# Kernel tuning notes

Hardware: AMD Instinct MI355X
Metric: run time of the kernel (lower is better)

## Reference

```python
import jax, jax.numpy as jnp
import numpy as np

N, F_IN, HID, C = 50000, 256, 64, 40
E = 1_600_000
EPS = 1e-8  # torch cosine_similarity eps


def setup_inputs() -> dict:
    key = jax.random.key(0)
    ks = jax.random.split(key, 6)
    x = jax.random.normal(ks[0], (N, F_IN), jnp.float32)
    edge_index = jax.random.randint(ks[1], (2, E), 0, N, dtype=jnp.int64)
    edge_weights = jax.random.uniform(ks[2], (E,), jnp.float32)
    W1 = jax.random.normal(ks[3], (F_IN, HID), jnp.float32) / np.float32(np.sqrt(F_IN))
    b1 = jnp.zeros((HID,), jnp.float32)
    W2 = jax.random.normal(ks[4], (HID, C), jnp.float32) / np.float32(np.sqrt(HID))
    b2 = jnp.zeros((C,), jnp.float32)
    return {"x": x, "edge_index": edge_index, "edge_weights": edge_weights,
            "W1": W1, "b1": b1, "W2": W2, "b2": b2}


def _gcn_conv(x, W, b, src, dst, n):
    # PyG GCNConv: out = D^{-1/2} (A + I) D^{-1/2} (X W) + b
    xw = x @ W  # [n, out]
    loops = jnp.arange(n, dtype=src.dtype)
    s = jnp.concatenate([src, loops])  # self-loops appended
    d = jnp.concatenate([dst, loops])
    deg = jax.ops.segment_sum(jnp.ones_like(s, dtype=xw.dtype), d, num_segments=n)
    dinv = jnp.where(deg > 0, jax.lax.rsqrt(jnp.maximum(deg, 1.0)), 0.0)
    norm = dinv[s] * dinv[d]  # [E+n]
    msg = xw[s] * norm[:, None]  # gather + scale (irregular access)
    out = jax.ops.segment_sum(msg, d, num_segments=n)  # scatter-add
    return out + b


def reference(x, edge_index, edge_weights, W1, b1, W2, b2):
    src, dst = edge_index[0], edge_index[1]
    n = x.shape[0]
    # layer 1 + relu (dropout = identity in eval)
    h = jax.nn.relu(_gcn_conv(x, W1, b1, src, dst, n))
    x_out = _gcn_conv(h, W2, b2, src, dst, n)  # [n, C]
    # edge-wise cosine dissimilarity: 1 - cos(x_out[src], x_out[dst])
    a = x_out[src]
    b = x_out[dst]
    na = jnp.maximum(jnp.sqrt(jnp.sum(a * a, axis=-1)), EPS)
    nb = jnp.maximum(jnp.sqrt(jnp.sum(b * b, axis=-1)), EPS)
    cosine_sim = 1.0 - jnp.sum(a * b, axis=-1) / (na * nb)
    gnn_edge = jnp.where(edge_weights > 0.5, 1.0, -1.0)
    return (jax.nn.log_softmax(x_out, axis=1), x_out, cosine_sim, gnn_edge,
            jax.nn.softmax(x_out, axis=1))
```

## Files before the change

### kernel.cpp

```cpp
#include <hip/hip_runtime.h>
#include <hip/hip_bf16.h>

#define F_IN 256
#define HID  64
#define CLS  40
#define EPS  1e-8f
#define XS_STRIDE 264
#define EPB  8192

typedef unsigned short ushort_t;
typedef unsigned int   uint_t;
typedef __attribute__((ext_vector_type(8))) short bf16x8;
typedef __attribute__((ext_vector_type(4))) float f32x4;

__device__ __forceinline__ float bf2f(ushort_t u) {
    union { uint_t i; float f; } v; v.i = ((uint_t)u) << 16; return v.f;
}
__device__ __forceinline__ ushort_t f2bf(float f) {
    union { float f; uint_t i; } v; v.f = f;
    uint_t r = v.i + 0x7fff + ((v.i >> 16) & 1);
    return (ushort_t)(r >> 16);
}
__device__ __forceinline__ float blo(uint_t p) {
    union { uint_t i; float f; } v; v.i = p << 16; return v.f;
}
__device__ __forceinline__ float bhi(uint_t p) {
    union { uint_t i; float f; } v; v.i = p & 0xffff0000u; return v.f;
}
__device__ __forceinline__ float dot_u4(uint4 a, uint4 b) {
    return blo(a.x) * blo(b.x) + bhi(a.x) * bhi(b.x)
         + blo(a.y) * blo(b.y) + bhi(a.y) * bhi(b.y)
         + blo(a.z) * blo(b.z) + bhi(a.z) * bhi(b.z)
         + blo(a.w) * blo(b.w) + bhi(a.w) * bhi(b.w);
}

__global__ void detect_kernel(const int* __restrict__ raw, int* __restrict__ flag) {
    int c = threadIdx.x;
    int w = raw[2 * c + 1];
    unsigned long long b = __ballot(w != 0);
    if (c == 0) *flag = (b == 0ULL) ? 1 : 0;
}

__global__ void build_hist_kernel(const void* __restrict__ raw, const int* __restrict__ flag,
                                  uint_t* __restrict__ pair, int* __restrict__ ghist, int E) {
    __shared__ int lhist[256];
    int tid = threadIdx.x;
    lhist[tid] = 0;
    __syncthreads();
    int base = blockIdx.x * EPB;
    if (*flag) {
        const long long* r = (const long long*)raw;
        for (int it = 0; it < EPB / 1024; ++it) {
            int e = base + (it * 256 + tid) * 4;
            if (e + 4 <= E) {
                ulonglong2 a0 = *(const ulonglong2*)(r + e);
                ulonglong2 a1 = *(const ulonglong2*)(r + e + 2);
                ulonglong2 b0 = *(const ulonglong2*)(r + E + e);
                ulonglong2 b1 = *(const ulonglong2*)(r + E + e + 2);
                uint_t d0 = (uint_t)b0.x, d1 = (uint_t)b0.y;
                uint_t d2 = (uint_t)b1.x, d3 = (uint_t)b1.y;
                uint4 p;
                p.x = (d0 << 16) | (uint_t)a0.x;
                p.y = (d1 << 16) | (uint_t)a0.y;
                p.z = (d2 << 16) | (uint_t)a1.x;
                p.w = (d3 << 16) | (uint_t)a1.y;
                *(uint4*)(pair + e) = p;
                atomicAdd(&lhist[d0 >> 8], 1);
                atomicAdd(&lhist[d1 >> 8], 1);
                atomicAdd(&lhist[d2 >> 8], 1);
                atomicAdd(&lhist[d3 >> 8], 1);
            } else {
                for (int k = 0; k < 4; ++k) {
                    int ee = e + k;
                    if (ee < E) {
                        uint_t s = (uint_t)r[ee];
                        uint_t d = (uint_t)r[E + ee];
                        pair[ee] = (d << 16) | s;
                        atomicAdd(&lhist[d >> 8], 1);
                    }
                }
            }
        }
    } else {
        const int* r = (const int*)raw;
        for (int it = 0; it < EPB / 1024; ++it) {
            int e = base + (it * 256 + tid) * 4;
            if (e + 4 <= E) {
                int4 a = *(const int4*)(r + e);
                int4 b = *(const int4*)(r + E + e);
                uint_t d0 = (uint_t)b.x, d1 = (uint_t)b.y;
                uint_t d2 = (uint_t)b.z, d3 = (uint_t)b.w;
                uint4 p;
                p.x = (d0 << 16) | (uint_t)a.x;
                p.y = (d1 << 16) | (uint_t)a.y;
                p.z = (d2 << 16) | (uint_t)a.z;
                p.w = (d3 << 16) | (uint_t)a.w;
                *(uint4*)(pair + e) = p;
                atomicAdd(&lhist[d0 >> 8], 1);
                atomicAdd(&lhist[d1 >> 8], 1);
                atomicAdd(&lhist[d2 >> 8], 1);
                atomicAdd(&lhist[d3 >> 8], 1);
            } else {
                for (int k = 0; k < 4; ++k) {
                    int ee = e + k;
                    if (ee < E) {
                        uint_t s = (uint_t)r[ee];
                        uint_t d = (uint_t)r[E + ee];
                        pair[ee] = (d << 16) | s;
                        atomicAdd(&lhist[d >> 8], 1);
                    }
                }
            }
        }
    }
    __syncthreads();
    ghist[blockIdx.x * 256 + tid] = lhist[tid];
}

__global__ void scan_cols_kernel(int* __restrict__ ghist, int* __restrict__ btot,
                                 int NBLK) {
    int k    = blockIdx.x;
    int lane = threadIdx.x;
    int carry = 0;
    for (int b0 = 0; b0 < NBLK; b0 += 64) {
        int b = b0 + lane;
        int v = (b < NBLK) ? ghist[b * 256 + k] : 0;
        int x = v;
        #pragma unroll
        for (int o = 1; o < 64; o <<= 1) {
            int t = __shfl_up(x, o);
            if (lane >= o) x += t;
        }
        if (b < NBLK) ghist[b * 256 + k] = carry + x - v;
        carry += __shfl(x, 63);
    }
    if (lane == 0) btot[k] = carry;
}

__global__ void scan_base_kernel(const int* __restrict__ btot, int* __restrict__ bbase) {
    __shared__ int s[256];
    int k = threadIdx.x;
    int v = btot[k];
    int x = v;
    s[k] = x;
    __syncthreads();
    #pragma unroll
    for (int o = 1; o < 256; o <<= 1) {
        int t = (k >= o) ? s[k - o] : 0;
        __syncthreads();
        x += t;
        s[k] = x;
        __syncthreads();
    }
    bbase[k] = x - v;
    if (k == 255) bbase[256] = x;
}

__global__ void scatter_buckets_kernel(const uint_t* __restrict__ pair,
                                       const int* __restrict__ ghist,
                                       const int* __restrict__ bbase,
                                       uint_t* __restrict__ bkt, int E) {
    __shared__ int cursor[256];
    int tid = threadIdx.x;
    cursor[tid] = ghist[blockIdx.x * 256 + tid] + bbase[tid];
    __syncthreads();
    int base = blockIdx.x * EPB;
    for (int it = 0; it < EPB / 256; ++it) {
        int e = base + it * 256 + tid;
        if (e < E) {
            uint_t u = pair[e];
            int pos = atomicAdd(&cursor[u >> 24], 1);
            bkt[pos] = u;
        }
    }
}

__global__ void bucket_csr_kernel(const uint_t* __restrict__ bkt,
                                  const int* __restrict__ bbase,
                                  ushort_t* __restrict__ csr, int* __restrict__ rowptr,
                                  float* __restrict__ dinv, int n, int E, int NBUCK) {
    __shared__ int lhist[256];
    __shared__ int lscan[256];
    __shared__ int cursor[256];
    int tid = threadIdx.x;
    int kb  = blockIdx.x;
    int base = bbase[kb];
    int cnt  = bbase[kb + 1] - base;
    lhist[tid] = 0;
    __syncthreads();
    for (int i = tid; i < cnt; i += 256) {
        uint_t u = bkt[base + i];
        atomicAdd(&lhist[(u >> 16) & 255], 1);
    }
    __syncthreads();
    int v = lhist[tid];
    int x = v;
    lscan[tid] = x;
    __syncthreads();
    #pragma unroll
    for (int o = 1; o < 256; o <<= 1) {
        int t = (tid >= o) ? lscan[tid - o] : 0;
        __syncthreads();
        x += t;
        lscan[tid] = x;
        __syncthreads();
    }
    int excl = x - v;
    int node = kb * 256 + tid;
    if (node < n) {
        rowptr[node] = base + excl;
        dinv[node]   = rsqrtf((float)(v + 1));
    }
    cursor[tid] = base + excl;
    if (kb == NBUCK - 1 && tid == 0) rowptr[n] = E;
    __syncthreads();
    for (int i = tid; i < cnt; i += 256) {
        uint_t u = bkt[base + i];
        int pos = atomicAdd(&cursor[(u >> 16) & 255], 1);
        csr[pos] = (ushort_t)(u & 0xffffu);
    }
}

__global__ void convert_w1_kernel(const float* __restrict__ W1, ushort_t* __restrict__ W1s) {
    int t = blockIdx.x * blockDim.x + threadIdx.x;
    if (t >= 4 * 8 * 64) return;
    int lane = t & 63;
    int kk   = (t >> 6) & 7;
    int nt   = t >> 9;
    int col  = nt * 16 + (lane & 15);
    int k0   = kk * 32 + (lane >> 4) * 8;
    ushort_t v[8];
    #pragma unroll
    for (int j = 0; j < 8; ++j) v[j] = f2bf(W1[(size_t)(k0 + j) * HID + col]);
    uint4 p;
    p.x = (uint_t)v[0] | ((uint_t)v[1] << 16);
    p.y = (uint_t)v[2] | ((uint_t)v[3] << 16);
    p.z = (uint_t)v[4] | ((uint_t)v[5] << 16);
    p.w = (uint_t)v[6] | ((uint_t)v[7] << 16);
    *(uint4*)(W1s + (size_t)t * 8) = p;
}

__global__ void gemm1_mfma_kernel(const float* __restrict__ x,
                                  const ushort_t* __restrict__ W1s,
                                  const float* __restrict__ dinv,
                                  ushort_t* __restrict__ xws, int n) {
    __shared__ ushort_t xs[16 * XS_STRIDE];
    int node0 = blockIdx.x * 16;
    int tid = threadIdx.x;
    for (int i = tid; i < 16 * 64; i += 256) {
        int r  = i >> 6;
        int c4 = (i & 63) << 2;
        int node = node0 + r;
        float4 v = (node < n) ? *(const float4*)(x + (size_t)node * F_IN + c4)
                              : make_float4(0.f, 0.f, 0.f, 0.f);
        ushort4 b;
        b.x = f2bf(v.x); b.y = f2bf(v.y); b.z = f2bf(v.z); b.w = f2bf(v.w);
        *(ushort4*)(&xs[r * XS_STRIDE + c4]) = b;
    }
    __syncthreads();
    int wave = tid >> 6;
    int lane = tid & 63;
    int m    = lane & 15;
    int q    = lane >> 4;
    f32x4 acc = {0.f, 0.f, 0.f, 0.f};
    #pragma unroll
    for (int kk = 0; kk < 8; ++kk) {
        bf16x8 a = *(const bf16x8*)(&xs[m * XS_STRIDE + kk * 32 + q * 8]);
        bf16x8 b = *(const bf16x8*)(W1s + (((size_t)wave * 8 + kk) * 64 + lane) * 8);
        acc = __builtin_amdgcn_mfma_f32_16x16x32_bf16(a, b, acc, 0, 0, 0);
    }
    int ch = wave * 16 + m;
    #pragma unroll
    for (int r = 0; r < 4; ++r) {
        int node = node0 + q * 4 + r;
        if (node < n)
            xws[(size_t)node * HID + ch] = f2bf(acc[r] * dinv[node]);
    }
}

__global__ void gather1_gemm2_kernel(const int* __restrict__ rowptr,
                                     const ushort_t* __restrict__ csr,
                                     const ushort_t* __restrict__ xws,
                                     const float* __restrict__ dinv,
                                     const float* __restrict__ b1,
                                     const float* __restrict__ W2,
                                     ushort_t* __restrict__ hws, int n) {
    __shared__ float hbuf[4][72];
    __shared__ float w2s[HID * CLS];
    int tid  = threadIdx.x;
    int wave = tid >> 6;
    int l    = tid & 63;
    int g    = l >> 3;
    int lc   = l & 7;
    for (int i = tid; i < HID * CLS / 4; i += 256)
        *(float4*)(&w2s[i * 4]) = *(const float4*)(W2 + i * 4);
    int wv = (blockIdx.x * blockDim.x + tid) >> 6;
    bool active = wv < n;
    int beg = 0, endp = 0;
    float di = 0.f;
    float acc8[8];
    #pragma unroll
    for (int j = 0; j < 8; ++j) acc8[j] = 0.f;
    if (active) {
        beg = rowptr[wv]; endp = rowptr[wv + 1];
        di  = dinv[wv];
        if (l < 8) {
            uint4 sv = *(const uint4*)(xws + (size_t)wv * HID + lc * 8);
            acc8[0] = blo(sv.x); acc8[1] = bhi(sv.x);
            acc8[2] = blo(sv.y); acc8[3] = bhi(sv.y);
            acc8[4] = blo(sv.z); acc8[5] = bhi(sv.z);
            acc8[6] = blo(sv.w); acc8[7] = bhi(sv.w);
        }
    }
    for (int ch = beg; ch < endp; ch += 32) {
        #pragma unroll
        for (int k = 0; k < 4; ++k) {
            int e = ch + k * 8 + g;
            bool val = e < endp;
            int ec = val ? e : (endp - 1);
            int s = (int)csr[ec];
            uint4 p = *(const uint4*)(xws + (size_t)s * HID + lc * 8);
            if (!val) { p.x = 0u; p.y = 0u; p.z = 0u; p.w = 0u; }
            acc8[0] += blo(p.x); acc8[1] += bhi(p.x);
            acc8[2] += blo(p.y); acc8[3] += bhi(p.y);
            acc8[4] += blo(p.z); acc8[5] += bhi(p.z);
            acc8[6] += blo(p.w); acc8[7] += bhi(p.w);
        }
    }
    #pragma unroll
    for (int j = 0; j < 8; ++j) {
        float v = acc8[j];
        v += __shfl_xor(v, 8);
        v += __shfl_xor(v, 16);
        v += __shfl_xor(v, 32);
        acc8[j] = v;
    }
    if (active && l < 8) {
        #pragma unroll
        for (int j = 0; j < 8; ++j)
            hbuf[wave][lc * 8 + j] = fmaxf(acc8[j] * di + b1[lc * 8 + j], 0.f);
    }
    __syncthreads();
    if (active) {
        if (l < CLS) {
            float o = 0.f;
            const float* hr = hbuf[wave];
            #pragma unroll 16
            for (int k = 0; k < HID; ++k) o += hr[k] * w2s[k * CLS + l];
            hws[(size_t)wv * HID + l] = f2bf(o * di);
        } else {
            hws[(size_t)wv * HID + l] = 0;
        }
    }
}

__global__ void gather2_fin_kernel(const int* __restrict__ rowptr,
                                   const ushort_t* __restrict__ csr,
                                   const ushort_t* __restrict__ hws,
                                   const float* __restrict__ dinv,
                                   const float* __restrict__ b2,
                                   float* __restrict__ xout, float* __restrict__ lsm,
                                   float* __restrict__ sm, ushort_t* __restrict__ xoutb,
                                   float* __restrict__ rnorm, int n) {
    int tid = threadIdx.x;
    int wv  = (blockIdx.x * blockDim.x + tid) >> 6;
    if (wv >= n) return;
    int l  = tid & 63;
    int g  = l >> 3;
    int lc = l & 7;
    int beg = rowptr[wv], endp = rowptr[wv + 1];
    float di = dinv[wv];
    float acc8[8];
    #pragma unroll
    for (int j = 0; j < 8; ++j) acc8[j] = 0.f;
    if (l < 8) {
        uint4 sv = *(const uint4*)(hws + (size_t)wv * HID + lc * 8);
        acc8[0] = blo(sv.x); acc8[1] = bhi(sv.x);
        acc8[2] = blo(sv.y); acc8[3] = bhi(sv.y);
        acc8[4] = blo(sv.z); acc8[5] = bhi(sv.z);
        acc8[6] = blo(sv.w); acc8[7] = bhi(sv.w);
    }
    for (int ch = beg; ch < endp; ch += 32) {
        #pragma unroll
        for (int k = 0; k < 4; ++k) {
            int e = ch + k * 8 + g;
            bool val = e < endp;
            int ec = val ? e : (endp - 1);
            int s = (int)csr[ec];
            uint4 p = *(const uint4*)(hws + (size_t)s * HID + lc * 8);
            if (!val) { p.x = 0u; p.y = 0u; p.z = 0u; p.w = 0u; }
            acc8[0] += blo(p.x); acc8[1] += bhi(p.x);
            acc8[2] += blo(p.y); acc8[3] += bhi(p.y);
            acc8[4] += blo(p.z); acc8[5] += bhi(p.z);
            acc8[6] += blo(p.w); acc8[7] += bhi(p.w);
        }
    }
    #pragma unroll
    for (int j = 0; j < 8; ++j) {
        float v = acc8[j];
        v += __shfl_xor(v, 8);
        v += __shfl_xor(v, 16);
        v += __shfl_xor(v, 32);
        acc8[j] = v;
    }
    bool cgv = lc < 5;
    float raw[8];
    if (cgv) {
        #pragma unroll
        for (int j = 0; j < 8; ++j) raw[j] = acc8[j] * di + b2[lc * 8 + j];
    } else {
        #pragma unroll
        for (int j = 0; j < 8; ++j) raw[j] = 0.f;
    }
    float mx = -3.0e38f;
    if (cgv) {
        #pragma unroll
        for (int j = 0; j < 8; ++j) mx = fmaxf(mx, raw[j]);
    }
    mx = fmaxf(mx, __shfl_xor(mx, 1));
    mx = fmaxf(mx, __shfl_xor(mx, 2));
    mx = fmaxf(mx, __shfl_xor(mx, 4));
    float ex[8];
    float ls = 0.f;
    if (cgv) {
        #pragma unroll
        for (int j = 0; j < 8; ++j) { ex[j] = __expf(raw[j] - mx); ls += ex[j]; }
    } else {
        #pragma unroll
        for (int j = 0; j < 8; ++j) ex[j] = 0.f;
    }
    ls += __shfl_xor(ls, 1);
    ls += __shfl_xor(ls, 2);
    ls += __shfl_xor(ls, 4);
    float sq = 0.f;
    if (cgv) {
        #pragma unroll
        for (int j = 0; j < 8; ++j) sq += raw[j] * raw[j];
    }
    sq += __shfl_xor(sq, 1);
    sq += __shfl_xor(sq, 2);
    sq += __shfl_xor(sq, 4);
    if (l < 5) {
        size_t fb = (size_t)wv * CLS + l * 8;
        *(float4*)(xout + fb)     = make_float4(raw[0], raw[1], raw[2], raw[3]);
        *(float4*)(xout + fb + 4) = make_float4(raw[4], raw[5], raw[6], raw[7]);
        float lse = mx + __logf(ls);
        *(float4*)(lsm + fb)     = make_float4(raw[0] - lse, raw[1] - lse, raw[2] - lse, raw[3] - lse);
        *(float4*)(lsm + fb + 4) = make_float4(raw[4] - lse, raw[5] - lse, raw[6] - lse, raw[7] - lse);
        float inv = 1.0f / ls;
        *(float4*)(sm + fb)     = make_float4(ex[0] * inv, ex[1] * inv, ex[2] * inv, ex[3] * inv);
        *(float4*)(sm + fb + 4) = make_float4(ex[4] * inv, ex[5] * inv, ex[6] * inv, ex[7] * inv);
        uint4 pb;
        pb.x = (uint_t)f2bf(raw[0]) | ((uint_t)f2bf(raw[1]) << 16);
        pb.y = (uint_t)f2bf(raw[2]) | ((uint_t)f2bf(raw[3]) << 16);
        pb.z = (uint_t)f2bf(raw[4]) | ((uint_t)f2bf(raw[5]) << 16);
        pb.w = (uint_t)f2bf(raw[6]) | ((uint_t)f2bf(raw[7]) << 16);
        *(uint4*)(xoutb + fb) = pb;
    }
    if (l == 0) rnorm[wv] = 1.0f / fmaxf(sqrtf(sq), EPS);
}

__global__ void edge_kernel(const uint_t* __restrict__ pair,
                            const float* __restrict__ ew, const ushort_t* __restrict__ xoutb,
                            const float* __restrict__ rnorm,
                            float* __restrict__ cos_out, float* __restrict__ gnn_out, int E) {
    int e = blockIdx.x * blockDim.x + threadIdx.x;
    if (e >= E) return;
    uint_t u = pair[e];
    int s = (int)(u & 0xffffu);
    int d = (int)(u >> 16);
    const uint4* a4 = (const uint4*)(xoutb + (size_t)s * CLS);
    const uint4* b4 = (const uint4*)(xoutb + (size_t)d * CLS);
    uint4 a0 = a4[0], a1 = a4[1], a2 = a4[2], a3 = a4[3], a4v = a4[4];
    uint4 b0 = b4[0], b1 = b4[1], b2 = b4[2], b3 = b4[3], b4v = b4[4];
    float rs = rnorm[s], rd = rnorm[d];
    float dot = dot_u4(a0, b0) + dot_u4(a1, b1) + dot_u4(a2, b2)
              + dot_u4(a3, b3) + dot_u4(a4v, b4v);
    cos_out[e] = 1.0f - dot * rs * rd;
    gnn_out[e] = (ew[e] > 0.5f) ? 1.0f : -1.0f;
}

extern "C" void kernel_launch(void* const* d_in, const int* in_sizes, int n_in,
                              void* d_out, int out_size, void* d_ws, size_t ws_size,
                              hipStream_t stream) {
    const float* x   = (const float*)d_in[0];
    const void*  ei  = d_in[1];
    const float* ew  = (const float*)d_in[2];
    const float* W1  = (const float*)d_in[3];
    const float* b1  = (const float*)d_in[4];
    const float* W2  = (const float*)d_in[5];
    const float* b2  = (const float*)d_in[6];

    const int n = in_sizes[0] / F_IN;
    const int E = in_sizes[2];

    float* lsm  = (float*)d_out;
    float* xout = lsm + (size_t)n * CLS;
    float* cosO = xout + (size_t)n * CLS;
    float* gnnO = cosO + E;
    float* smO  = gnnO + E;

    char* w = (char*)d_ws;
    auto alloc = [&](size_t bytes) {
        char* p = w;
        w += (bytes + 255) & ~(size_t)255;
        return p;
    };
    const int NBLK  = (E + EPB - 1) / EPB;
    const int NBUCK = (n + 255) / 256;

    uint_t*   pair   = (uint_t*)  alloc((size_t)E * 4);
    uint_t*   bkt    = (uint_t*)  alloc((size_t)E * 4);
    ushort_t* csr16  = (ushort_t*)alloc((size_t)E * 2);
    int*      ghist  = (int*)     alloc((size_t)NBLK * 256 * 4);
    int*      btot   = (int*)     alloc(256 * 4);
    int*      bbase  = (int*)     alloc(257 * 4);
    int*      rowptr = (int*)     alloc(((size_t)n + 1) * 4);
    float*    dinv   = (float*)   alloc((size_t)n * 4);
    ushort_t* xws    = (ushort_t*)alloc((size_t)n * HID * 2);
    ushort_t* hws    = (ushort_t*)alloc((size_t)n * HID * 2);
    ushort_t* xoutb  = (ushort_t*)alloc((size_t)n * CLS * 2);
    float*    rnorm  = (float*)   alloc((size_t)n * 4);
    ushort_t* W1s    = (ushort_t*)alloc((size_t)4 * 8 * 64 * 8 * 2);
    int*      flag   = (int*)     alloc(64);

    detect_kernel<<<1, 64, 0, stream>>>((const int*)ei, flag);
    convert_w1_kernel<<<8, 256, 0, stream>>>(W1, W1s);
    build_hist_kernel<<<NBLK, 256, 0, stream>>>(ei, flag, pair, ghist, E);
    scan_cols_kernel<<<256, 64, 0, stream>>>(ghist, btot, NBLK);
    scan_base_kernel<<<1, 256, 0, stream>>>(btot, bbase);
    scatter_buckets_kernel<<<NBLK, 256, 0, stream>>>(pair, ghist, bbase, bkt, E);
    bucket_csr_kernel<<<NBUCK, 256, 0, stream>>>(bkt, bbase, csr16, rowptr, dinv, n, E, NBUCK);
    gemm1_mfma_kernel<<<(n + 15) / 16, 256, 0, stream>>>(x, W1s, dinv, xws, n);
    gather1_gemm2_kernel<<<((size_t)n * 64 + 255) / 256, 256, 0, stream>>>(rowptr, csr16, xws, dinv,
                                                                           b1, W2, hws, n);
    gather2_fin_kernel<<<((size_t)n * 64 + 255) / 256, 256, 0, stream>>>(rowptr, csr16, hws, dinv, b2,
                                                                         xout, lsm, smO, xoutb, rnorm, n);
    edge_kernel<<<(E + 255) / 256, 256, 0, stream>>>(pair, ew, xoutb, rnorm, cosO, gnnO, E);
}
```

Baseline: 308.7 us.

## Pre-normalize bf16 node outputs and split edge dot product across 8 lanes

The finalize kernel now multiplies each node's output row by its reciprocal norm before packing it to bf16. This drops the separate rnorm array and the two per-edge norm lookups. The edge kernel now gives each edge 8 lanes: each lane loads one 16-byte chunk of the src and dst rows and the partial dots are reduced with shuffles. The aim is better memory-level parallelism and coalescing on the random gathers, at the cost of 8x more threads, three idle lanes per group and shuffle overhead.

```diff
diff --git a/kernel.cpp b/kernel.cpp
--- a/kernel.cpp
+++ b/kernel.cpp
@@ -360,8 +360,8 @@
                                    const float* __restrict__ dinv,
                                    const float* __restrict__ b2,
                                    float* __restrict__ xout, float* __restrict__ lsm,
-                                   float* __restrict__ sm, ushort_t* __restrict__ xoutb,
-                                   float* __restrict__ rnorm, int n) {
+                                   float* __restrict__ sm, ushort_t* __restrict__ xnb,
+                                   int n) {
     int tid = threadIdx.x;
     int wv  = (blockIdx.x * blockDim.x + tid) >> 6;
     if (wv >= n) return;
@@ -440,6 +440,7 @@
     sq += __shfl_xor(sq, 1);
     sq += __shfl_xor(sq, 2);
     sq += __shfl_xor(sq, 4);
+    float rn = 1.0f / fmaxf(sqrtf(sq), EPS);
     if (l < 5) {
         size_t fb = (size_t)wv * CLS + l * 8;
         *(float4*)(xout + fb)     = make_float4(raw[0], raw[1], raw[2], raw[3]);
@@ -451,33 +452,40 @@
         *(float4*)(sm + fb)     = make_float4(ex[0] * inv, ex[1] * inv, ex[2] * inv, ex[3] * inv);
         *(float4*)(sm + fb + 4) = make_float4(ex[4] * inv, ex[5] * inv, ex[6] * inv, ex[7] * inv);
         uint4 pb;
-        pb.x = (uint_t)f2bf(raw[0]) | ((uint_t)f2bf(raw[1]) << 16);
-        pb.y = (uint_t)f2bf(raw[2]) | ((uint_t)f2bf(raw[3]) << 16);
-        pb.z = (uint_t)f2bf(raw[4]) | ((uint_t)f2bf(raw[5]) << 16);
-        pb.w = (uint_t)f2bf(raw[6]) | ((uint_t)f2bf(raw[7]) << 16);
-        *(uint4*)(xoutb + fb) = pb;
-    }
-    if (l == 0) rnorm[wv] = 1.0f / fmaxf(sqrtf(sq), EPS);
+        pb.x = (uint_t)f2bf(raw[0] * rn) | ((uint_t)f2bf(raw[1] * rn) << 16);
+        pb.y = (uint_t)f2bf(raw[2] * rn) | ((uint_t)f2bf(raw[3] * rn) << 16);
+        pb.z = (uint_t)f2bf(raw[4] * rn) | ((uint_t)f2bf(raw[5] * rn) << 16);
+        pb.w = (uint_t)f2bf(raw[6] * rn) | ((uint_t)f2bf(raw[7] * rn) << 16);
+        *(uint4*)(xnb + fb) = pb;
+    }
 }
 
 __global__ void edge_kernel(const uint_t* __restrict__ pair,
-                            const float* __restrict__ ew, const ushort_t* __restrict__ xoutb,
-                            const float* __restrict__ rnorm,
+                            const float* __restrict__ ew, const ushort_t* __restrict__ xnb,
                             float* __restrict__ cos_out, float* __restrict__ gnn_out, int E) {
-    int e = blockIdx.x * blockDim.x + threadIdx.x;
+    int tid = threadIdx.x;
+    int wid = (blockIdx.x * blockDim.x + tid) >> 6;
+    int l = tid & 63;
+    int g = l >> 3;
+    int j = l & 7;
+    int e = wid * 8 + g;
     if (e >= E) return;
     uint_t u = pair[e];
     int s = (int)(u & 0xffffu);
     int d = (int)(u >> 16);
-    const uint4* a4 = (const uint4*)(xoutb + (size_t)s * CLS);
-    const uint4* b4 = (const uint4*)(xoutb + (size_t)d * CLS);
-    uint4 a0 = a4[0], a1 = a4[1], a2 = a4[2], a3 = a4[3], a4v = a4[4];
-    uint4 b0 = b4[0], b1 = b4[1], b2 = b4[2], b3 = b4[3], b4v = b4[4];
-    float rs = rnorm[s], rd = rnorm[d];
-    float dot = dot_u4(a0, b0) + dot_u4(a1, b1) + dot_u4(a2, b2)
-              + dot_u4(a3, b3) + dot_u4(a4v, b4v);
-    cos_out[e] = 1.0f - dot * rs * rd;
-    gnn_out[e] = (ew[e] > 0.5f) ? 1.0f : -1.0f;
+    float part = 0.f;
+    if (j < 5) {
+        uint4 a = *(const uint4*)(xnb + (size_t)s * CLS + j * 8);
+        uint4 b = *(const uint4*)(xnb + (size_t)d * CLS + j * 8);
+        part = dot_u4(a, b);
+    }
+    part += __shfl_xor(part, 1);
+    part += __shfl_xor(part, 2);
+    part += __shfl_xor(part, 4);
+    if (j == 0) {
+        cos_out[e] = 1.0f - part;
+        gnn_out[e] = (ew[e] > 0.5f) ? 1.0f : -1.0f;
+    }
 }
 
 extern "C" void kernel_launch(void* const* d_in, const int* in_sizes, int n_in,
@@ -519,8 +527,7 @@
     float*    dinv   = (float*)   alloc((size_t)n * 4);
     ushort_t* xws    = (ushort_t*)alloc((size_t)n * HID * 2);
     ushort_t* hws    = (ushort_t*)alloc((size_t)n * HID * 2);
-    ushort_t* xoutb  = (ushort_t*)alloc((size_t)n * CLS * 2);
-    float*    rnorm  = (float*)   alloc((size_t)n * 4);
+    ushort_t* xnb    = (ushort_t*)alloc((size_t)n * CLS * 2);
     ushort_t* W1s    = (ushort_t*)alloc((size_t)4 * 8 * 64 * 8 * 2);
     int*      flag   = (int*)     alloc(64);
 
@@ -535,6 +542,6 @@
     gather1_gemm2_kernel<<<((size_t)n * 64 + 255) / 256, 256, 0, stream>>>(rowptr, csr16, xws, dinv,
                                                                            b1, W2, hws, n);
     gather2_fin_kernel<<<((size_t)n * 64 + 255) / 256, 256, 0, stream>>>(rowptr, csr16, hws, dinv, b2,
-                                                                         xout, lsm, smO, xoutb, rnorm, n);
-    edge_kernel<<<(E + 255) / 256, 256, 0, stream>>>(pair, ew, xoutb, rnorm, cosO, gnnO, E);
-}
+                                                                         xout, lsm, smO, xnb, n);
+    edge_kernel<<<((size_t)E * 8 + 255) / 256, 256, 0, stream>>>(pair, ew, xnb, cosO, gnnO, E);
+}
```

Result: faster. 295.1 us (-4.4%).
